# Kernel tuning notes

Hardware: AMD Instinct MI355X
Metric: run time of the kernel (lower is better)

Reference implementation:

```python
import jax, jax.numpy as jnp
import numpy as np

EMBED_DIM = 768
NUM_HEADS = 12
HEAD_DIM = EMBED_DIM // NUM_HEADS


def setup_inputs() -> dict:
    key = jax.random.key(0)
    ks = jax.random.split(key, 9)
    B, N, D = 8, 1024, EMBED_DIM
    s = 1.0 / np.sqrt(D)
    x = jax.random.normal(ks[0], (B, N, D), dtype=jnp.float32)
    Wq = jax.random.normal(ks[1], (D, D), dtype=jnp.float32) * s
    bq = jnp.zeros((D,), dtype=jnp.float32)
    Wk = jax.random.normal(ks[2], (D, D), dtype=jnp.float32) * s
    bk = jnp.zeros((D,), dtype=jnp.float32)
    Wv = jax.random.normal(ks[3], (D, D), dtype=jnp.float32) * s
    bv = jnp.zeros((D,), dtype=jnp.float32)
    Wo = jax.random.normal(ks[4], (D, D), dtype=jnp.float32) * s
    bo = jnp.zeros((D,), dtype=jnp.float32)
    return {"x": x, "Wq": Wq, "bq": bq, "Wk": Wk, "bk": bk,
            "Wv": Wv, "bv": bv, "Wo": Wo, "bo": bo}


def reference(x, Wq, bq, Wk, bk, Wv, bv, Wo, bo):
    B, N, D = x.shape
    H, Hd = NUM_HEADS, HEAD_DIM
    # torch Linear: y = x @ W.T + b
    q = (x @ Wq.T + bq).reshape(B, N, H, Hd).transpose(0, 2, 1, 3)  # [B,H,N,Hd]
    k = (x @ Wk.T + bk).reshape(B, N, H, Hd).transpose(0, 2, 1, 3)
    v = (x @ Wv.T + bv).reshape(B, N, H, Hd).transpose(0, 2, 1, 3)
    # NOTE: original scales by embed_dim**-0.5 (not head_dim)
    scale = jnp.asarray(D, x.dtype) ** -0.5
    scores = jnp.einsum('bhnd,bhmd->bhnm', q, k) * scale  # [B,H,N,N]
    attn = jax.nn.softmax(scores, axis=-1)
    out = jnp.einsum('bhnm,bhmd->bhnd', attn, v)  # dropout: identity in eval
    out = out.transpose(0, 2, 1, 3).reshape(B, N, D)
    return out @ Wo.T + bo
```

## Files before the change

kernel.cpp:

```cpp
#include <hip/hip_runtime.h>
#include <math.h>


typedef __bf16 bf16x8 __attribute__((ext_vector_type(8)));
typedef float  f32x4  __attribute__((ext_vector_type(4)));
typedef unsigned u32x2 __attribute__((ext_vector_type(2)));
typedef unsigned u32x4 __attribute__((ext_vector_type(4)));
typedef unsigned short ushort_t;

__device__ __forceinline__ unsigned short f2bf(float f) {
    unsigned u = __float_as_uint(f);
    u += 0x7fffu + ((u >> 16) & 1u);
    return (unsigned short)(u >> 16);
}
__device__ __forceinline__ unsigned pk16(unsigned short lo, unsigned short hi) {
    return (unsigned)lo | ((unsigned)hi << 16);
}

__global__ __launch_bounds__(256)
void cast_all(const float* __restrict__ x,
              const float* __restrict__ w0, const float* __restrict__ w1,
              const float* __restrict__ w2, const float* __restrict__ w3,
              ushort_t* __restrict__ xb, ushort_t* __restrict__ wb0,
              ushort_t* __restrict__ wb1, ushort_t* __restrict__ wb2,
              ushort_t* __restrict__ wb3)
{
    const int wt0 = blockIdx.x * 4 + (threadIdx.x >> 6);
    const int L = threadIdx.x & 63, c = L & 15, g = L >> 4;
    const float* s; ushort_t* d; int tile;
    if (wt0 < 12288) {
        s = x; d = xb; tile = wt0;
    } else {
        const int wt = wt0 - 12288;
        const int wsel = wt / 1152; tile = wt % 1152;
        switch (wsel) {
            case 0:  s = w0; d = wb0; break;
            case 1:  s = w1; d = wb1; break;
            case 2:  s = w2; d = wb2; break;
            default: s = w3; d = wb3; break;
        }
    }
    const int t = tile / 24, kb = tile % 24;
    const float* sp = s + (size_t)(t * 16 + c) * 768 + kb * 32 + g * 8;
    const float4 f0 = *(const float4*)sp;
    const float4 f1 = *(const float4*)(sp + 4);
    ushort4 p0, p1;
    p0.x = f2bf(f0.x); p0.y = f2bf(f0.y); p0.z = f2bf(f0.z); p0.w = f2bf(f0.w);
    p1.x = f2bf(f1.x); p1.y = f2bf(f1.y); p1.z = f2bf(f1.z); p1.w = f2bf(f1.w);
    ushort_t* dp = d + ((size_t)tile * 64 + L) * 8;
    *(ushort4*)dp       = p0;
    *(ushort4*)(dp + 4) = p1;
}

__global__ __launch_bounds__(256, 3)
void gemm_qkv(const ushort_t* __restrict__ xb,
              const ushort_t* __restrict__ wqb, const ushort_t* __restrict__ wkb,
              const ushort_t* __restrict__ wvb,
              const float* __restrict__ bq, const float* __restrict__ bk,
              const float* __restrict__ bv,
              ushort_t* __restrict__ Qh, ushort_t* __restrict__ Kl,
              ushort_t* __restrict__ Vl)
{
    __shared__ ushort_t smem[9216];
    const int tid = threadIdx.x, L = tid & 63, wv = tid >> 6;
    const int c = L & 15, g = L >> 4;
    const int bid = blockIdx.x;
    const int xcd = bid & 7, idx = bid >> 3;
    const int by = xcd * 16 + idx / 6, bx = idx % 6;
    const int n0 = bx * 128, m0 = by * 64;

    const ushort_t* ap = xb + (size_t)(by * 4) * 24 * 512 + (size_t)L * 8;
    const size_t wbase = ((size_t)(bx * 8 + wv * 2) * 24 * 64 + L) * 8;
    const ushort_t* wqp = wqb + wbase;
    const ushort_t* wkp = wkb + wbase;
    const ushort_t* wvp = wvb + wbase;

    f32x4 acc[3][4][2];
#pragma unroll
    for (int z = 0; z < 3; ++z)
#pragma unroll
        for (int i = 0; i < 4; ++i)
#pragma unroll
            for (int j = 0; j < 2; ++j) acc[z][i][j] = (f32x4){0.f, 0.f, 0.f, 0.f};

    bf16x8 af[4], wf[3][2];
#pragma unroll
    for (int i = 0; i < 4; ++i) af[i] = *(const bf16x8*)(ap + i * 12288);
#pragma unroll
    for (int j = 0; j < 2; ++j) {
        wf[0][j] = *(const bf16x8*)(wqp + j * 12288);
        wf[1][j] = *(const bf16x8*)(wkp + j * 12288);
        wf[2][j] = *(const bf16x8*)(wvp + j * 12288);
    }

    for (int kb = 0; kb < 24; ++kb) {
#pragma unroll
        for (int z = 0; z < 3; ++z)
#pragma unroll
            for (int i = 0; i < 4; ++i)
#pragma unroll
                for (int j = 0; j < 2; ++j)
                    acc[z][i][j] = __builtin_amdgcn_mfma_f32_16x16x32_bf16(
                        af[i], wf[z][j], acc[z][i][j], 0, 0, 0);
        const int kn = (kb < 23) ? kb + 1 : 23;
#pragma unroll
        for (int i = 0; i < 4; ++i)
            af[i] = *(const bf16x8*)(ap + i * 12288 + kn * 512);
#pragma unroll
        for (int j = 0; j < 2; ++j) {
            wf[0][j] = *(const bf16x8*)(wqp + j * 12288 + kn * 512);
            wf[1][j] = *(const bf16x8*)(wkp + j * 12288 + kn * 512);
            wf[2][j] = *(const bf16x8*)(wvp + j * 12288 + kn * 512);
        }
    }

    const int b  = m0 >> 10, nb = m0 & 1023;
    const int hcol = n0 + wv * 32;
    const int h = hcol >> 6, uh = (hcol >> 5) & 1;
    const int bh = b * 12 + h;
    ushort_t* scr = smem + wv * 2304;

    float bias2[3][2];
#pragma unroll
    for (int j = 0; j < 2; ++j) {
        bias2[0][j] = bq[hcol + j * 16 + c];
        bias2[1][j] = bk[hcol + j * 16 + c];
        bias2[2][j] = bv[hcol + j * 16 + c];
    }

#pragma unroll
    for (int i = 0; i < 4; ++i)
#pragma unroll
        for (int j = 0; j < 2; ++j)
#pragma unroll
            for (int r = 0; r < 4; ++r)
                scr[(i * 16 + g * 4 + r) * 36 + j * 16 + c] =
                    f2bf(acc[0][i][j][r] + bias2[0][j]);
#pragma unroll
    for (int e = 0; e < 4; ++e) {
        const int slot = e * 64 + L;
        const int row = slot >> 2, ch = slot & 3;
        const u32x4 v = *(const u32x4*)&scr[row * 36 + ch * 8];
        *(u32x4*)&Qh[((size_t)bh * 1024 + nb + row) * 64 + uh * 32 + ch * 8] = v;
    }

#pragma unroll
    for (int i = 0; i < 4; ++i)
#pragma unroll
        for (int j = 0; j < 2; ++j)
#pragma unroll
            for (int r = 0; r < 4; ++r)
                scr[(i * 16 + g * 4 + r) * 36 + j * 16 + c] =
                    f2bf(acc[1][i][j][r] + bias2[1][j]);
#pragma unroll
    for (int tau = 0; tau < 4; ++tau) {
        const u32x4 v = *(const u32x4*)&scr[(tau * 16 + c) * 36 + g * 8];
        *(u32x4*)&Kl[(((size_t)bh * 64 + (nb >> 4) + tau) * 2 + uh) * 512
                     + (size_t)L * 8] = v;
    }

#pragma unroll
    for (int i = 0; i < 4; ++i)
#pragma unroll
        for (int j = 0; j < 2; ++j)
#pragma unroll
            for (int r = 0; r < 4; ++r)
                scr[(j * 16 + c) * 68 + i * 16 + g * 4 + r] =
                    f2bf(acc[2][i][j][r] + bias2[2][j]);
    const int T = nb >> 6;
#pragma unroll
    for (int t = 0; t < 4; ++t) {
        const int htl = t >> 1, u = t & 1;
        const u32x4 v = *(const u32x4*)&scr[(htl * 16 + c) * 68 + u * 32 + g * 8];
        *(u32x4*)&Vl[((((size_t)bh * 4 + uh * 2 + htl) * 16 + T) * 2 + u) * 512
                     + (size_t)L * 8] = v;
    }
}

__global__ __launch_bounds__(256, 3)
void gemm_outp(const ushort_t* __restrict__ attnb, const ushort_t* __restrict__ wob,
               const float* __restrict__ bo, float* __restrict__ out)
{
    const int tid = threadIdx.x, L = tid & 63, wv = tid >> 6;
    const int c = L & 15, g = L >> 4;
    const int bid = blockIdx.x;
    const int xcd = bid & 7, idx = bid >> 3;
    const int by = xcd * 16 + idx / 6, bx = idx % 6;
    const int n0 = bx * 128, m0 = by * 64;

    const ushort_t* ap = attnb + (size_t)(by * 4) * 24 * 512 + (size_t)L * 8;
    const size_t wbase = ((size_t)(bx * 8 + wv * 2) * 24 * 64 + L) * 8;
    const ushort_t* wop = wob + wbase;

    f32x4 acc[4][2];
#pragma unroll
    for (int i = 0; i < 4; ++i)
#pragma unroll
        for (int j = 0; j < 2; ++j) acc[i][j] = (f32x4){0.f, 0.f, 0.f, 0.f};

    bf16x8 af[4], wf[2];
#pragma unroll
    for (int i = 0; i < 4; ++i) af[i] = *(const bf16x8*)(ap + i * 12288);
#pragma unroll
    for (int j = 0; j < 2; ++j) wf[j] = *(const bf16x8*)(wop + j * 12288);

    for (int kb = 0; kb < 24; ++kb) {
#pragma unroll
        for (int i = 0; i < 4; ++i)
#pragma unroll
            for (int j = 0; j < 2; ++j)
                acc[i][j] = __builtin_amdgcn_mfma_f32_16x16x32_bf16(
                    af[i], wf[j], acc[i][j], 0, 0, 0);
        const int kn = (kb < 23) ? kb + 1 : 23;
#pragma unroll
        for (int i = 0; i < 4; ++i)
            af[i] = *(const bf16x8*)(ap + i * 12288 + kn * 512);
#pragma unroll
        for (int j = 0; j < 2; ++j)
            wf[j] = *(const bf16x8*)(wop + j * 12288 + kn * 512);
    }

#pragma unroll
    for (int i = 0; i < 4; ++i) {
        const int row = m0 + i * 16 + g * 4;
#pragma unroll
        for (int j = 0; j < 2; ++j) {
            const int col = n0 + wv * 32 + j * 16 + c;
            const float bsvo = bo[col];
#pragma unroll
            for (int r = 0; r < 4; ++r)
                out[(size_t)(row + r) * 768 + col] = acc[i][j][r] + bsvo;
        }
    }
}

__global__ __launch_bounds__(64, 3)
void flash_bf16(const ushort_t* __restrict__ Q, const ushort_t* __restrict__ Kl,
                const ushort_t* __restrict__ Vl, ushort_t* __restrict__ attnb)
{
    __shared__ ushort_t Ps[2][2][16 * 68];
    const int L = threadIdx.x;
    const int c = L & 15, g = L >> 4;
    const int bid = blockIdx.x;
    const int slot = bid >> 3;
    const int bh = (bid & 7) * 12 + (slot >> 5);
    const int q0 = (slot & 31) * 32;
    const float SC2 = 0.05205954985329743f;

    const ushort_t* Qp = Q + ((size_t)bh * 1024 + q0 + c) * 64 + g * 8;
    bf16x8 qf[2][2];
    qf[0][0] = *(const bf16x8*)Qp;
    qf[0][1] = *(const bf16x8*)(Qp + 32);
    qf[1][0] = *(const bf16x8*)(Qp + 16 * 64);
    qf[1][1] = *(const bf16x8*)(Qp + 16 * 64 + 32);

    const ushort_t* Kb = Kl + (size_t)bh * 65536 + (size_t)L * 8;
    const ushort_t* Vb = Vl + (size_t)bh * 65536 + (size_t)L * 8;

    f32x4 o[2][4];
#pragma unroll
    for (int w = 0; w < 2; ++w)
#pragma unroll
        for (int ht = 0; ht < 4; ++ht) o[w][ht] = (f32x4){0.f, 0.f, 0.f, 0.f};
    float ls[2] = {0.f, 0.f};

    bf16x8 kf0[4], kf1[4];
#pragma unroll
    for (int ct = 0; ct < 4; ++ct) {
        kf0[ct] = *(const bf16x8*)(Kb + (size_t)(ct * 2 + 0) * 512);
        kf1[ct] = *(const bf16x8*)(Kb + (size_t)(ct * 2 + 1) * 512);
    }

    for (int T0 = 0; T0 < 16; T0 += 2) {
#pragma unroll
        for (int p = 0; p < 2; ++p) {
            const int T = T0 + p;
            bf16x8 vf0[4], vf1[4];
#pragma unroll
            for (int ht = 0; ht < 4; ++ht) {
                const ushort_t* vp = Vb + (size_t)((ht * 16 + T) * 2) * 512;
                vf0[ht] = *(const bf16x8*)vp;
                vf1[ht] = *(const bf16x8*)(vp + 512);
            }
            f32x4 s[2][4];
#pragma unroll
            for (int w = 0; w < 2; ++w)
#pragma unroll
                for (int ct = 0; ct < 4; ++ct) {
                    f32x4 zz = (f32x4){0.f, 0.f, 0.f, 0.f};
                    zz = __builtin_amdgcn_mfma_f32_16x16x32_bf16(kf0[ct], qf[w][0], zz, 0, 0, 0);
                    zz = __builtin_amdgcn_mfma_f32_16x16x32_bf16(kf1[ct], qf[w][1], zz, 0, 0, 0);
                    s[w][ct] = zz;
                }
            const int Tn = (T < 15) ? T + 1 : 15;
#pragma unroll
            for (int ct = 0; ct < 4; ++ct) {
                const ushort_t* kp = Kb + (size_t)((Tn * 4 + ct) * 2) * 512;
                kf0[ct] = *(const bf16x8*)kp;
                kf1[ct] = *(const bf16x8*)(kp + 512);
            }
#pragma unroll
            for (int w = 0; w < 2; ++w) {
#pragma unroll
                for (int ct = 0; ct < 4; ++ct) {
                    float pv[4];
#pragma unroll
                    for (int r = 0; r < 4; ++r)
                        pv[r] = __builtin_amdgcn_exp2f(s[w][ct][r] * SC2);
                    ls[w] += (pv[0] + pv[1]) + (pv[2] + pv[3]);
                    const unsigned w01 = __builtin_amdgcn_perm(
                        __float_as_uint(pv[1]), __float_as_uint(pv[0]), 0x07060302u);
                    const unsigned w23 = __builtin_amdgcn_perm(
                        __float_as_uint(pv[3]), __float_as_uint(pv[2]), 0x07060302u);
                    *(u32x2*)&Ps[p][w][c * 68 + ct * 16 + g * 4] = (u32x2){w01, w23};
                }
            }
#pragma unroll
            for (int w = 0; w < 2; ++w) {
                const int pb = c * 68 + g * 8;
                const u32x4 pa  = *(const u32x4*)&Ps[p][w][pb];
                const u32x4 pbv = *(const u32x4*)&Ps[p][w][pb + 32];
                const bf16x8 pf0 = __builtin_bit_cast(bf16x8, pa);
                const bf16x8 pf1 = __builtin_bit_cast(bf16x8, pbv);
#pragma unroll
                for (int ht = 0; ht < 4; ++ht) {
                    o[w][ht] = __builtin_amdgcn_mfma_f32_16x16x32_bf16(vf0[ht], pf0, o[w][ht], 0, 0, 0);
                    o[w][ht] = __builtin_amdgcn_mfma_f32_16x16x32_bf16(vf1[ht], pf1, o[w][ht], 0, 0, 0);
                }
            }
        }
    }

    const int b = bh / 12, h = bh % 12;
    const int tB = b * 64 + (q0 >> 4);
#pragma unroll
    for (int w = 0; w < 2; ++w) {
        float l = ls[w];
        l += __shfl_xor(l, 16);
        l += __shfl_xor(l, 32);
        const float inv = 1.f / l;
#pragma unroll
        for (int ht = 0; ht < 4; ++ht) {
            const unsigned w0 = pk16(f2bf(o[w][ht][0] * inv), f2bf(o[w][ht][1] * inv));
            const unsigned w1 = pk16(f2bf(o[w][ht][2] * inv), f2bf(o[w][ht][3] * inv));
            *(u32x2*)&Ps[0][w][c * 68 + ht * 16 + g * 4] = (u32x2){w0, w1};
        }
#pragma unroll
        for (int kbi = 0; kbi < 2; ++kbi) {
            const u32x4 v = *(const u32x4*)&Ps[0][w][c * 68 + kbi * 32 + g * 8];
            *(u32x4*)&attnb[(((size_t)(tB + w) * 24 + h * 2 + kbi) * 64 + L) * 8] = v;
        }
    }
}

extern "C" void kernel_launch(void* const* d_in, const int* in_sizes, int n_in,
                              void* d_out, int out_size, void* d_ws, size_t ws_size,
                              hipStream_t stream)
{
    const float* x  = (const float*)d_in[0];
    const float* Wq = (const float*)d_in[1];
    const float* bq = (const float*)d_in[2];
    const float* Wk = (const float*)d_in[3];
    const float* bk = (const float*)d_in[4];
    const float* Wv = (const float*)d_in[5];
    const float* bv = (const float*)d_in[6];
    const float* Wo = (const float*)d_in[7];
    const float* bo = (const float*)d_in[8];
    float* out = (float*)d_out;

    char* ws = (char*)d_ws;
    ushort_t* xb    = (ushort_t*)(ws);
    ushort_t* wqb   = (ushort_t*)(ws + 12582912);
    ushort_t* wkb   = (ushort_t*)(ws + 12582912 + 1179648);
    ushort_t* wvb   = (ushort_t*)(ws + 12582912 + 2359296);
    ushort_t* wob   = (ushort_t*)(ws + 12582912 + 3538944);
    ushort_t* Qh    = (ushort_t*)(ws + 17301504);
    ushort_t* Kl    = (ushort_t*)(ws + 29884416);
    ushort_t* Vl    = (ushort_t*)(ws + 42467328);
    ushort_t* attnb = (ushort_t*)(ws + 55050240);

    cast_all<<<dim3(4224), 256, 0, stream>>>(x, Wq, Wk, Wv, Wo,
                                             xb, wqb, wkb, wvb, wob);
    gemm_qkv<<<dim3(768), 256, 0, stream>>>(xb, wqb, wkb, wvb,
                                            bq, bk, bv, Qh, Kl, Vl);
    flash_bf16<<<dim3(3072), 64, 0, stream>>>(Qh, Kl, Vl, attnb);
    gemm_outp<<<dim3(768), 256, 0, stream>>>(attnb, wob, bo, out);
}
```

Baseline: 180.6 us.

## Split flash attention block's two query tiles across two wavefronts

The flash kernel now launches 128 threads per block, with each wavefront handling one 16-row query tile instead of a single wave handling both. This halves per-wave register use (accumulators, scores, Q fragments), which should improve occupancy and latency hiding. In exchange, each wave loads the same K and V fragments separately, doubling global/L2 read traffic for K/V per block. The shared P buffer is indexed by wave, so no extra sync is needed.

```diff
diff --git a/kernel.cpp b/kernel.cpp
--- a/kernel.cpp
+++ b/kernel.cpp
@@ -234,35 +234,32 @@
     }
 }
 
-__global__ __launch_bounds__(64, 3)
+__global__ __launch_bounds__(128, 3)
 void flash_bf16(const ushort_t* __restrict__ Q, const ushort_t* __restrict__ Kl,
                 const ushort_t* __restrict__ Vl, ushort_t* __restrict__ attnb)
 {
     __shared__ ushort_t Ps[2][2][16 * 68];
-    const int L = threadIdx.x;
+    const int tid = threadIdx.x;
+    const int L = tid & 63, w = tid >> 6;
     const int c = L & 15, g = L >> 4;
     const int bid = blockIdx.x;
     const int slot = bid >> 3;
     const int bh = (bid & 7) * 12 + (slot >> 5);
-    const int q0 = (slot & 31) * 32;
+    const int q0 = (slot & 31) * 32 + w * 16;
     const float SC2 = 0.05205954985329743f;
 
     const ushort_t* Qp = Q + ((size_t)bh * 1024 + q0 + c) * 64 + g * 8;
-    bf16x8 qf[2][2];
-    qf[0][0] = *(const bf16x8*)Qp;
-    qf[0][1] = *(const bf16x8*)(Qp + 32);
-    qf[1][0] = *(const bf16x8*)(Qp + 16 * 64);
-    qf[1][1] = *(const bf16x8*)(Qp + 16 * 64 + 32);
+    bf16x8 qf[2];
+    qf[0] = *(const bf16x8*)Qp;
+    qf[1] = *(const bf16x8*)(Qp + 32);
 
     const ushort_t* Kb = Kl + (size_t)bh * 65536 + (size_t)L * 8;
     const ushort_t* Vb = Vl + (size_t)bh * 65536 + (size_t)L * 8;
 
-    f32x4 o[2][4];
-#pragma unroll
-    for (int w = 0; w < 2; ++w)
-#pragma unroll
-        for (int ht = 0; ht < 4; ++ht) o[w][ht] = (f32x4){0.f, 0.f, 0.f, 0.f};
-    float ls[2] = {0.f, 0.f};
+    f32x4 o[4];
+#pragma unroll
+    for (int ht = 0; ht < 4; ++ht) o[ht] = (f32x4){0.f, 0.f, 0.f, 0.f};
+    float ls = 0.f;
 
     bf16x8 kf0[4], kf1[4];
 #pragma unroll
@@ -282,16 +279,14 @@
                 vf0[ht] = *(const bf16x8*)vp;
                 vf1[ht] = *(const bf16x8*)(vp + 512);
             }
-            f32x4 s[2][4];
-#pragma unroll
-            for (int w = 0; w < 2; ++w)
-#pragma unroll
-                for (int ct = 0; ct < 4; ++ct) {
-                    f32x4 zz = (f32x4){0.f, 0.f, 0.f, 0.f};
-                    zz = __builtin_amdgcn_mfma_f32_16x16x32_bf16(kf0[ct], qf[w][0], zz, 0, 0, 0);
-                    zz = __builtin_amdgcn_mfma_f32_16x16x32_bf16(kf1[ct], qf[w][1], zz, 0, 0, 0);
-                    s[w][ct] = zz;
-                }
+            f32x4 s[4];
+#pragma unroll
+            for (int ct = 0; ct < 4; ++ct) {
+                f32x4 zz = (f32x4){0.f, 0.f, 0.f, 0.f};
+                zz = __builtin_amdgcn_mfma_f32_16x16x32_bf16(kf0[ct], qf[0], zz, 0, 0, 0);
+                zz = __builtin_amdgcn_mfma_f32_16x16x32_bf16(kf1[ct], qf[1], zz, 0, 0, 0);
+                s[ct] = zz;
+            }
             const int Tn = (T < 15) ? T + 1 : 15;
 #pragma unroll
             for (int ct = 0; ct < 4; ++ct) {
@@ -300,23 +295,19 @@
                 kf1[ct] = *(const bf16x8*)(kp + 512);
             }
 #pragma unroll
-            for (int w = 0; w < 2; ++w) {
-#pragma unroll
-                for (int ct = 0; ct < 4; ++ct) {
-                    float pv[4];
-#pragma unroll
-                    for (int r = 0; r < 4; ++r)
-                        pv[r] = __builtin_amdgcn_exp2f(s[w][ct][r] * SC2);
-                    ls[w] += (pv[0] + pv[1]) + (pv[2] + pv[3]);
-                    const unsigned w01 = __builtin_amdgcn_perm(
-                        __float_as_uint(pv[1]), __float_as_uint(pv[0]), 0x07060302u);
-                    const unsigned w23 = __builtin_amdgcn_perm(
-                        __float_as_uint(pv[3]), __float_as_uint(pv[2]), 0x07060302u);
-                    *(u32x2*)&Ps[p][w][c * 68 + ct * 16 + g * 4] = (u32x2){w01, w23};
-                }
-            }
-#pragma unroll
-            for (int w = 0; w < 2; ++w) {
+            for (int ct = 0; ct < 4; ++ct) {
+                float pv[4];
+#pragma unroll
+                for (int r = 0; r < 4; ++r)
+                    pv[r] = __builtin_amdgcn_exp2f(s[ct][r] * SC2);
+                ls += (pv[0] + pv[1]) + (pv[2] + pv[3]);
+                const unsigned w01 = __builtin_amdgcn_perm(
+                    __float_as_uint(pv[1]), __float_as_uint(pv[0]), 0x07060302u);
+                const unsigned w23 = __builtin_amdgcn_perm(
+                    __float_as_uint(pv[3]), __float_as_uint(pv[2]), 0x07060302u);
+                *(u32x2*)&Ps[p][w][c * 68 + ct * 16 + g * 4] = (u32x2){w01, w23};
+            }
+            {
                 const int pb = c * 68 + g * 8;
                 const u32x4 pa  = *(const u32x4*)&Ps[p][w][pb];
                 const u32x4 pbv = *(const u32x4*)&Ps[p][w][pb + 32];
@@ -324,8 +315,8 @@
                 const bf16x8 pf1 = __builtin_bit_cast(bf16x8, pbv);
 #pragma unroll
                 for (int ht = 0; ht < 4; ++ht) {
-                    o[w][ht] = __builtin_amdgcn_mfma_f32_16x16x32_bf16(vf0[ht], pf0, o[w][ht], 0, 0, 0);
-                    o[w][ht] = __builtin_amdgcn_mfma_f32_16x16x32_bf16(vf1[ht], pf1, o[w][ht], 0, 0, 0);
+                    o[ht] = __builtin_amdgcn_mfma_f32_16x16x32_bf16(vf0[ht], pf0, o[ht], 0, 0, 0);
+                    o[ht] = __builtin_amdgcn_mfma_f32_16x16x32_bf16(vf1[ht], pf1, o[ht], 0, 0, 0);
                 }
             }
         }
@@ -333,22 +324,21 @@
 
     const int b = bh / 12, h = bh % 12;
     const int tB = b * 64 + (q0 >> 4);
-#pragma unroll
-    for (int w = 0; w < 2; ++w) {
-        float l = ls[w];
+    {
+        float l = ls;
         l += __shfl_xor(l, 16);
         l += __shfl_xor(l, 32);
         const float inv = 1.f / l;
 #pragma unroll
         for (int ht = 0; ht < 4; ++ht) {
-            const unsigned w0 = pk16(f2bf(o[w][ht][0] * inv), f2bf(o[w][ht][1] * inv));
-            const unsigned w1 = pk16(f2bf(o[w][ht][2] * inv), f2bf(o[w][ht][3] * inv));
+            const unsigned w0 = pk16(f2bf(o[ht][0] * inv), f2bf(o[ht][1] * inv));
+            const unsigned w1 = pk16(f2bf(o[ht][2] * inv), f2bf(o[ht][3] * inv));
             *(u32x2*)&Ps[0][w][c * 68 + ht * 16 + g * 4] = (u32x2){w0, w1};
         }
 #pragma unroll
         for (int kbi = 0; kbi < 2; ++kbi) {
             const u32x4 v = *(const u32x4*)&Ps[0][w][c * 68 + kbi * 32 + g * 8];
-            *(u32x4*)&attnb[(((size_t)(tB + w) * 24 + h * 2 + kbi) * 64 + L) * 8] = v;
+            *(u32x4*)&attnb[(((size_t)tB * 24 + h * 2 + kbi) * 64 + L) * 8] = v;
         }
     }
 }
@@ -383,6 +373,6 @@
                                              xb, wqb, wkb, wvb, wob);
     gemm_qkv<<<dim3(768), 256, 0, stream>>>(xb, wqb, wkb, wvb,
                                             bq, bk, bv, Qh, Kl, Vl);
-    flash_bf16<<<dim3(3072), 64, 0, stream>>>(Qh, Kl, Vl, attnb);
+    flash_bf16<<<dim3(3072), 128, 0, stream>>>(Qh, Kl, Vl, attnb);
     gemm_outp<<<dim3(768), 256, 0, stream>>>(attnb, wob, bo, out);
 }
```

Measured after the change: 207.2 us. +14.7%, slower.

## Split flash attention KV loop across two waves with shared-memory reduction

Applied to the files above, without the earlier changes.

Each flash block now runs two waves, and each wave processes half of the key/value tiles for the same 32 queries. The partial outputs and row sums are then combined through shared memory before normalisation and the bf16 store. Splitting the serial KV loop across waves doubles the wave count per block, which should raise latency hiding and MFMA utilisation. In exchange it adds a block barrier, an fp32 shared-memory reduction and more LDS per block.

```diff
diff --git a/kernel.cpp b/kernel.cpp
--- a/kernel.cpp
+++ b/kernel.cpp
@@ -234,12 +234,13 @@
     }
 }
 
-__global__ __launch_bounds__(64, 3)
+__global__ __launch_bounds__(128, 3)
 void flash_bf16(const ushort_t* __restrict__ Q, const ushort_t* __restrict__ Kl,
                 const ushort_t* __restrict__ Vl, ushort_t* __restrict__ attnb)
 {
-    __shared__ ushort_t Ps[2][2][16 * 68];
-    const int L = threadIdx.x;
+    __shared__ ushort_t smem[6528];
+    const int tid = threadIdx.x;
+    const int L = tid & 63, w = tid >> 6;
     const int c = L & 15, g = L >> 4;
     const int bid = blockIdx.x;
     const int slot = bid >> 3;
@@ -257,99 +258,119 @@
     const ushort_t* Kb = Kl + (size_t)bh * 65536 + (size_t)L * 8;
     const ushort_t* Vb = Vl + (size_t)bh * 65536 + (size_t)L * 8;
 
+    ushort_t* st0 = smem + (w * 2 + 0) * 1088;
+    ushort_t* st1 = smem + (w * 2 + 1) * 1088;
+
     f32x4 o[2][4];
 #pragma unroll
-    for (int w = 0; w < 2; ++w)
-#pragma unroll
-        for (int ht = 0; ht < 4; ++ht) o[w][ht] = (f32x4){0.f, 0.f, 0.f, 0.f};
+    for (int u = 0; u < 2; ++u)
+#pragma unroll
+        for (int ht = 0; ht < 4; ++ht) o[u][ht] = (f32x4){0.f, 0.f, 0.f, 0.f};
     float ls[2] = {0.f, 0.f};
 
+    const int Tbeg = w * 8;
     bf16x8 kf0[4], kf1[4];
 #pragma unroll
     for (int ct = 0; ct < 4; ++ct) {
-        kf0[ct] = *(const bf16x8*)(Kb + (size_t)(ct * 2 + 0) * 512);
-        kf1[ct] = *(const bf16x8*)(Kb + (size_t)(ct * 2 + 1) * 512);
-    }
-
-    for (int T0 = 0; T0 < 16; T0 += 2) {
-#pragma unroll
-        for (int p = 0; p < 2; ++p) {
-            const int T = T0 + p;
-            bf16x8 vf0[4], vf1[4];
+        const ushort_t* kp = Kb + (size_t)((Tbeg * 4 + ct) * 2) * 512;
+        kf0[ct] = *(const bf16x8*)kp;
+        kf1[ct] = *(const bf16x8*)(kp + 512);
+    }
+
+#pragma unroll 2
+    for (int T = Tbeg; T < Tbeg + 8; ++T) {
+        bf16x8 vf0[4], vf1[4];
+#pragma unroll
+        for (int ht = 0; ht < 4; ++ht) {
+            const ushort_t* vp = Vb + (size_t)((ht * 16 + T) * 2) * 512;
+            vf0[ht] = *(const bf16x8*)vp;
+            vf1[ht] = *(const bf16x8*)(vp + 512);
+        }
+        f32x4 s[2][4];
+#pragma unroll
+        for (int u = 0; u < 2; ++u)
+#pragma unroll
+            for (int ct = 0; ct < 4; ++ct) {
+                f32x4 zz = (f32x4){0.f, 0.f, 0.f, 0.f};
+                zz = __builtin_amdgcn_mfma_f32_16x16x32_bf16(kf0[ct], qf[u][0], zz, 0, 0, 0);
+                zz = __builtin_amdgcn_mfma_f32_16x16x32_bf16(kf1[ct], qf[u][1], zz, 0, 0, 0);
+                s[u][ct] = zz;
+            }
+        const int Tn = (T < Tbeg + 7) ? T + 1 : T;
+#pragma unroll
+        for (int ct = 0; ct < 4; ++ct) {
+            const ushort_t* kp = Kb + (size_t)((Tn * 4 + ct) * 2) * 512;
+            kf0[ct] = *(const bf16x8*)kp;
+            kf1[ct] = *(const bf16x8*)(kp + 512);
+        }
+#pragma unroll
+        for (int u = 0; u < 2; ++u) {
+            ushort_t* st = u ? st1 : st0;
+#pragma unroll
+            for (int ct = 0; ct < 4; ++ct) {
+                float pv[4];
+#pragma unroll
+                for (int r = 0; r < 4; ++r)
+                    pv[r] = __builtin_amdgcn_exp2f(s[u][ct][r] * SC2);
+                ls[u] += (pv[0] + pv[1]) + (pv[2] + pv[3]);
+                const unsigned w01 = __builtin_amdgcn_perm(
+                    __float_as_uint(pv[1]), __float_as_uint(pv[0]), 0x07060302u);
+                const unsigned w23 = __builtin_amdgcn_perm(
+                    __float_as_uint(pv[3]), __float_as_uint(pv[2]), 0x07060302u);
+                *(u32x2*)&st[c * 68 + ct * 16 + g * 4] = (u32x2){w01, w23};
+            }
+        }
+#pragma unroll
+        for (int u = 0; u < 2; ++u) {
+            const ushort_t* st = u ? st1 : st0;
+            const int pb = c * 68 + g * 8;
+            const u32x4 pa  = *(const u32x4*)&st[pb];
+            const u32x4 pbv = *(const u32x4*)&st[pb + 32];
+            const bf16x8 pf0 = __builtin_bit_cast(bf16x8, pa);
+            const bf16x8 pf1 = __builtin_bit_cast(bf16x8, pbv);
 #pragma unroll
             for (int ht = 0; ht < 4; ++ht) {
-                const ushort_t* vp = Vb + (size_t)((ht * 16 + T) * 2) * 512;
-                vf0[ht] = *(const bf16x8*)vp;
-                vf1[ht] = *(const bf16x8*)(vp + 512);
+                o[u][ht] = __builtin_amdgcn_mfma_f32_16x16x32_bf16(vf0[ht], pf0, o[u][ht], 0, 0, 0);
+                o[u][ht] = __builtin_amdgcn_mfma_f32_16x16x32_bf16(vf1[ht], pf1, o[u][ht], 0, 0, 0);
             }
-            f32x4 s[2][4];
-#pragma unroll
-            for (int w = 0; w < 2; ++w)
-#pragma unroll
-                for (int ct = 0; ct < 4; ++ct) {
-                    f32x4 zz = (f32x4){0.f, 0.f, 0.f, 0.f};
-                    zz = __builtin_amdgcn_mfma_f32_16x16x32_bf16(kf0[ct], qf[w][0], zz, 0, 0, 0);
-                    zz = __builtin_amdgcn_mfma_f32_16x16x32_bf16(kf1[ct], qf[w][1], zz, 0, 0, 0);
-                    s[w][ct] = zz;
-                }
-            const int Tn = (T < 15) ? T + 1 : 15;
-#pragma unroll
-            for (int ct = 0; ct < 4; ++ct) {
-                const ushort_t* kp = Kb + (size_t)((Tn * 4 + ct) * 2) * 512;
-                kf0[ct] = *(const bf16x8*)kp;
-                kf1[ct] = *(const bf16x8*)(kp + 512);
-            }
-#pragma unroll
-            for (int w = 0; w < 2; ++w) {
-#pragma unroll
-                for (int ct = 0; ct < 4; ++ct) {
-                    float pv[4];
-#pragma unroll
-                    for (int r = 0; r < 4; ++r)
-                        pv[r] = __builtin_amdgcn_exp2f(s[w][ct][r] * SC2);
-                    ls[w] += (pv[0] + pv[1]) + (pv[2] + pv[3]);
-                    const unsigned w01 = __builtin_amdgcn_perm(
-                        __float_as_uint(pv[1]), __float_as_uint(pv[0]), 0x07060302u);
-                    const unsigned w23 = __builtin_amdgcn_perm(
-                        __float_as_uint(pv[3]), __float_as_uint(pv[2]), 0x07060302u);
-                    *(u32x2*)&Ps[p][w][c * 68 + ct * 16 + g * 4] = (u32x2){w01, w23};
-                }
-            }
-#pragma unroll
-            for (int w = 0; w < 2; ++w) {
-                const int pb = c * 68 + g * 8;
-                const u32x4 pa  = *(const u32x4*)&Ps[p][w][pb];
-                const u32x4 pbv = *(const u32x4*)&Ps[p][w][pb + 32];
-                const bf16x8 pf0 = __builtin_bit_cast(bf16x8, pa);
-                const bf16x8 pf1 = __builtin_bit_cast(bf16x8, pbv);
-#pragma unroll
-                for (int ht = 0; ht < 4; ++ht) {
-                    o[w][ht] = __builtin_amdgcn_mfma_f32_16x16x32_bf16(vf0[ht], pf0, o[w][ht], 0, 0, 0);
-                    o[w][ht] = __builtin_amdgcn_mfma_f32_16x16x32_bf16(vf1[ht], pf1, o[w][ht], 0, 0, 0);
-                }
-            }
         }
     }
 
     const int b = bh / 12, h = bh % 12;
+    float* oF  = (float*)smem;
+    float* lsF = oF + 2048;
+    const int uo = 1 - w;
+
+    __syncthreads();
+#pragma unroll
+    for (int ht = 0; ht < 4; ++ht)
+#pragma unroll
+        for (int r = 0; r < 4; ++r)
+            oF[w * 1024 + (ht * 4 + r) * 64 + L] = o[uo][ht][r];
+    lsF[w * 64 + L] = ls[uo];
+    __syncthreads();
+
+    float l = ls[w] + lsF[uo * 64 + L];
+    l += __shfl_xor(l, 16);
+    l += __shfl_xor(l, 32);
+    const float inv = 1.f / l;
+
+    ushort_t* strip = smem + 4352 + w * 1088;
+#pragma unroll
+    for (int ht = 0; ht < 4; ++ht) {
+        const float v0 = o[w][ht][0] + oF[uo * 1024 + (ht * 4 + 0) * 64 + L];
+        const float v1 = o[w][ht][1] + oF[uo * 1024 + (ht * 4 + 1) * 64 + L];
+        const float v2 = o[w][ht][2] + oF[uo * 1024 + (ht * 4 + 2) * 64 + L];
+        const float v3 = o[w][ht][3] + oF[uo * 1024 + (ht * 4 + 3) * 64 + L];
+        const unsigned w0 = pk16(f2bf(v0 * inv), f2bf(v1 * inv));
+        const unsigned w1 = pk16(f2bf(v2 * inv), f2bf(v3 * inv));
+        *(u32x2*)&strip[c * 68 + ht * 16 + g * 4] = (u32x2){w0, w1};
+    }
     const int tB = b * 64 + (q0 >> 4);
 #pragma unroll
-    for (int w = 0; w < 2; ++w) {
-        float l = ls[w];
-        l += __shfl_xor(l, 16);
-        l += __shfl_xor(l, 32);
-        const float inv = 1.f / l;
-#pragma unroll
-        for (int ht = 0; ht < 4; ++ht) {
-            const unsigned w0 = pk16(f2bf(o[w][ht][0] * inv), f2bf(o[w][ht][1] * inv));
-            const unsigned w1 = pk16(f2bf(o[w][ht][2] * inv), f2bf(o[w][ht][3] * inv));
-            *(u32x2*)&Ps[0][w][c * 68 + ht * 16 + g * 4] = (u32x2){w0, w1};
-        }
-#pragma unroll
-        for (int kbi = 0; kbi < 2; ++kbi) {
-            const u32x4 v = *(const u32x4*)&Ps[0][w][c * 68 + kbi * 32 + g * 8];
-            *(u32x4*)&attnb[(((size_t)(tB + w) * 24 + h * 2 + kbi) * 64 + L) * 8] = v;
-        }
+    for (int kbi = 0; kbi < 2; ++kbi) {
+        const u32x4 v = *(const u32x4*)&strip[c * 68 + kbi * 32 + g * 8];
+        *(u32x4*)&attnb[(((size_t)(tB + w) * 24 + h * 2 + kbi) * 64 + L) * 8] = v;
     }
 }
 
@@ -383,6 +404,6 @@
                                              xb, wqb, wkb, wvb, wob);
     gemm_qkv<<<dim3(768), 256, 0, stream>>>(xb, wqb, wkb, wvb,
                                             bq, bk, bv, Qh, Kl, Vl);
-    flash_bf16<<<dim3(3072), 64, 0, stream>>>(Qh, Kl, Vl, attnb);
+    flash_bf16<<<dim3(3072), 128, 0, stream>>>(Qh, Kl, Vl, attnb);
     gemm_outp<<<dim3(768), 256, 0, stream>>>(attnb, wob, bo, out);
 }
```

Result: slower. 226.7 us (+25.5%).
